# Optimization experiments

Measured on AMD Instinct MI355X. Metric: run time of the kernel, lower is better.

Reference implementation:

```python
import jax, jax.numpy as jnp
import numpy as np

B, T, N, E = 4, 8, 3000, 12000
D = 256; H = 256; HEADS = 8; DH = H // HEADS; F = 8; L = 3; HD = 64
NEG_SLOPE = 0.2


def layer_norm(x, g, b):
    m = x.mean(-1, keepdims=True)
    v = x.var(-1, keepdims=True)
    return (x - m) / jnp.sqrt(v + 1e-5) * g + b


def gat(x, edge_emb, src, dst, W, We, a_src, a_dst, a_edge):
    # x: [B,N,Din], edge_emb: [B,E,H] -> [B,N,H] via edge-conditioned graph attention
    Bc, Nc = x.shape[0], x.shape[1]
    xw = (x @ W).reshape(Bc, Nc, HEADS, DH)
    ew = (edge_emb @ We).reshape(Bc, -1, HEADS, DH)
    xs = xw[:, src]  # [B,E,HEADS,DH] gather
    xd = xw[:, dst]
    logit = (xs * a_src).sum(-1) + (xd * a_dst).sum(-1) + (ew * a_edge).sum(-1)  # [B,E,HEADS]
    logit = jnp.where(logit > 0, logit, NEG_SLOPE * logit)  # leaky_relu(0.2)

    def seg_softmax(lg):  # softmax over incoming edges per dst node
        m = jax.ops.segment_max(lg, dst, num_segments=Nc)
        e = jnp.exp(lg - m[dst])
        s = jax.ops.segment_sum(e, dst, num_segments=Nc)
        return e / (s[dst] + 1e-16)

    w = jax.vmap(seg_softmax)(logit)  # [B,E,HEADS]
    msg = (xs + ew) * w[..., None]
    out = jax.vmap(lambda m_: jax.ops.segment_sum(m_, dst, num_segments=Nc))(msg)
    return out.reshape(Bc, Nc, H)


def mlp(x, w1, b1, w2, b2):
    return jax.nn.relu(x @ w1 + b1) @ w2 + b2


def setup_inputs() -> dict:
    key = jax.random.key(0)
    ks = iter(jax.random.split(key, 64))
    rn = lambda s, sc=1.0: jax.random.normal(next(ks), s, dtype=jnp.float32) * sc
    return {
        'env_emb': rn((B, T, N, D)), 'infra_emb': rn((B, T, N, D)), 'robot_emb': rn((B, T, N, D)),
        'edge_attr': rn((B, E, F)),
        'edge_index': jax.random.randint(next(ks), (2, E), 0, N),
        'wqkv': rn((D, 3 * D), 0.05), 'bqkv': jnp.zeros((3 * D,), jnp.float32),
        'wo': rn((D, D), 0.05), 'bo': jnp.zeros((D,), jnp.float32),
        'lnf_g': jnp.ones((D,), jnp.float32), 'lnf_b': jnp.zeros((D,), jnp.float32),
        'we_emb': rn((F, H), 0.1), 'be_emb': jnp.zeros((H,), jnp.float32),
        'tg_W': rn((D, H), 0.05), 'tg_We': rn((H, H), 0.05),
        'tg_asrc': rn((HEADS, DH), 0.1), 'tg_adst': rn((HEADS, DH), 0.1), 'tg_aedge': rn((HEADS, DH), 0.1),
        'w_ih': rn((H, 4 * H), 0.05), 'w_hh': rn((H, 4 * H), 0.05), 'b_lstm': jnp.zeros((4 * H,), jnp.float32),
        'g_W': rn((L, H, H), 0.05), 'g_We': rn((L, H, H), 0.05),
        'g_asrc': rn((L, HEADS, DH), 0.1), 'g_adst': rn((L, HEADS, DH), 0.1), 'g_aedge': rn((L, HEADS, DH), 0.1),
        'g_lng': jnp.ones((L, H), jnp.float32), 'g_lnb': jnp.zeros((L, H), jnp.float32),
        'hn_w1': rn((8, H, HD), 0.05), 'hn_b1': jnp.zeros((8, HD), jnp.float32),
        'hn_w2': rn((8, HD, 1), 0.05), 'hn_b2': jnp.zeros((8, 1), jnp.float32),
        'he_w1': rn((2, 2 * H, HD), 0.05), 'he_b1': jnp.zeros((2, HD), jnp.float32),
        'he_w2': rn((2, HD, 1), 0.05), 'he_b2': jnp.zeros((2, 1), jnp.float32),
    }


def reference(env_emb, infra_emb, robot_emb, edge_attr, edge_index,
              wqkv, bqkv, wo, bo, lnf_g, lnf_b, we_emb, be_emb,
              tg_W, tg_We, tg_asrc, tg_adst, tg_aedge,
              w_ih, w_hh, b_lstm,
              g_W, g_We, g_asrc, g_adst, g_aedge, g_lng, g_lnb,
              hn_w1, hn_b1, hn_w2, hn_b2, he_w1, he_b1, he_w2, he_b2):
    # --- per-timestep 3-token cross-modal self-attention, vectorized over B,T,N ---
    tokens = jnp.stack([env_emb, infra_emb, robot_emb], axis=3)  # [B,T,N,3,D]
    qkv = tokens @ wqkv + bqkv
    q, k, v = jnp.split(qkv, 3, axis=-1)
    sh = tokens.shape[:-1] + (HEADS, DH)
    q = q.reshape(sh); k = k.reshape(sh); v = v.reshape(sh)
    att = jax.nn.softmax(jnp.einsum('btnqhd,btnkhd->btnhqk', q, k) / np.sqrt(DH).astype(np.float32), axis=-1)
    o = jnp.einsum('btnhqk,btnkhd->btnqhd', att, v).reshape(tokens.shape)
    fused_seq = layer_norm((o @ wo + bo).mean(axis=3), lnf_g, lnf_b)  # [B,T,N,D]

    edge_emb = jax.nn.relu(edge_attr @ we_emb + be_emb)  # [B,E,H]
    src = edge_index[0]; dst = edge_index[1]

    # --- TemporalGNNCell: GAT message passing feeding an LSTM cell, scanned over T ---
    def step(carry, x_t):
        h, c = carry
        m = gat(x_t, edge_emb, src, dst, tg_W, tg_We, tg_asrc, tg_adst, tg_aedge)
        gates = m @ w_ih + h @ w_hh + b_lstm
        i, f, g, oo = jnp.split(gates, 4, axis=-1)
        c = jax.nn.sigmoid(f) * c + jax.nn.sigmoid(i) * jnp.tanh(g)
        h = jax.nn.sigmoid(oo) * jnp.tanh(c)
        return (h, c), None

    z = jnp.zeros((B, N, H), fused_seq.dtype)
    (h, _), _ = jax.lax.scan(step, (z, z), jnp.moveaxis(fused_seq, 1, 0))

    # --- stacked residual GAT layers with LayerNorm ---
    for i in range(L):
        h_new = gat(h, edge_emb, src, dst, g_W[i], g_We[i], g_asrc[i], g_adst[i], g_aedge[i])
        h = layer_norm(h + h_new, g_lng[i], g_lnb[i])

    # --- prediction heads ---
    failure = jax.nn.sigmoid(mlp(h, hn_w1[0], hn_b1[0], hn_w2[0], hn_b2[0]))
    timing = jax.nn.softplus(mlp(h, hn_w1[1], hn_b1[1], hn_w2[1], hn_b2[1]))
    others = [mlp(h, hn_w1[j], hn_b1[j], hn_w2[j], hn_b2[j]) for j in range(2, 6)]  # voltage, angle, temperature, reactive
    risk = jax.nn.sigmoid(mlp(h, hn_w1[6], hn_b1[6], hn_w2[6], hn_b2[6]))
    node_out = jnp.concatenate([failure, timing] + others + [risk], axis=-1)  # [B,N,7]
    h_global = h.mean(axis=1, keepdims=True)
    freq = mlp(h_global, hn_w1[7], hn_b1[7], hn_w2[7], hn_b2[7]).reshape(B, 1)
    ef = jnp.concatenate([h[:, src], h[:, dst]], axis=-1)  # [B,E,2H]
    line = mlp(ef, he_w1[0], he_b1[0], he_w2[0], he_b2[0])
    active = mlp(ef, he_w1[1], he_b1[1], he_w2[1], he_b2[1])
    return jnp.concatenate([node_out.reshape(B, -1), line.reshape(B, -1), active.reshape(B, -1), freq], axis=1)
```

## Files before the change

kernel.cpp:

```cpp
#include <hip/hip_runtime.h>
#include <hip/hip_bf16.h>
#include <math.h>

#define DEV __device__ __forceinline__

namespace {
constexpr int B_ = 4, T_ = 8, N_ = 3000, E_ = 12000;
constexpr int OUTS_ = 45001;
}

using f32x4 = __attribute__((ext_vector_type(4))) float;
using bf16x8 = __attribute__((ext_vector_type(8))) short;

DEV float sigm_(float x) { return 1.0f / (1.0f + expf(-x)); }
DEV float softplus_(float x) { return fmaxf(x, 0.0f) + log1pf(expf(-fabsf(x))); }
DEV float wred_(float v) {
  #pragma unroll
  for (int o = 32; o > 0; o >>= 1) v += __shfl_xor(v, o, 64);
  return v;
}
DEV unsigned short f2bf(float x) {
  unsigned u = __float_as_uint(x);
  return (unsigned short)((u + 0x7FFFu + ((u >> 16) & 1u)) >> 16);
}
DEV unsigned f2bf2(float a, float b) {
  return (unsigned)f2bf(a) | ((unsigned)f2bf(b) << 16);
}
DEV float bfl(unsigned u) { return __uint_as_float(u << 16); }
DEV float bfh(unsigned u) { return __uint_as_float(u & 0xffff0000u); }

__global__ void wtb_k(const float* __restrict__ W, unsigned short* __restrict__ Wt,
                      int K, int N, int total)
{
  const int idx = blockIdx.x * blockDim.x + threadIdx.x;
  if (idx >= total) return;
  const int kn = K * N;
  const int l = idx / kn;
  const int r = idx - l * kn;
  const int k = r / N, n = r - k * N;
  Wt[(size_t)l * kn + (size_t)n * K + k] = f2bf(W[idx]);
}

__global__ void wtp_k(const float* __restrict__ W, unsigned short* __restrict__ Wt,
                      int kOff)
{
  const int idx = blockIdx.x * blockDim.x + threadIdx.x;
  if (idx >= 256 * 1024) return;
  const int k = idx >> 10;
  const int n = idx & 1023;
  const int newcol = (n & 255) * 4 + (n >> 8);
  Wt[(size_t)newcol * 512 + kOff + k] = f2bf(W[idx]);
}

__global__ void hist_k(const int* __restrict__ dst, int* __restrict__ deg)
{
  const int e = blockIdx.x * blockDim.x + threadIdx.x;
  if (e < E_) atomicAdd(&deg[dst[e]], 1);
}

__global__ __launch_bounds__(256) void scan_k(const int* __restrict__ deg,
                                              int* __restrict__ roff)
{
  __shared__ int part[256];
  const int t = threadIdx.x;
  int loc[12];
  int s = 0;
  #pragma unroll
  for (int i = 0; i < 12; ++i) {
    const int n = t * 12 + i;
    loc[i] = s;
    s += (n < N_) ? deg[n] : 0;
  }
  part[t] = s;
  __syncthreads();
  if (t == 0) {
    int run = 0;
    for (int i = 0; i < 256; ++i) { const int v = part[i]; part[i] = run; run += v; }
  }
  __syncthreads();
  const int base = part[t];
  #pragma unroll
  for (int i = 0; i < 12; ++i) {
    const int n = t * 12 + i;
    if (n < N_) roff[n] = base + loc[i];
  }
  if (t == 0) roff[N_] = E_;
}

__global__ __launch_bounds__(256) void fill_k(const int* __restrict__ dst,
                                              const int* __restrict__ roff,
                                              int* __restrict__ eord)
{
  const int n = blockIdx.x * 4 + (threadIdx.x >> 6);
  if (n >= N_) return;
  const int lane = threadIdx.x & 63;
  const unsigned long long ltm = (1ull << lane) - 1ull;
  int cnt = roff[n];
  for (int c = 0; c < E_; c += 64) {
    const int e = c + lane;
    const bool m = (e < E_) && (dst[e] == n);
    const unsigned long long mask = __ballot(m);
    if (m) eord[cnt + __popcll(mask & ltm)] = e;
    cnt += __popcll(mask);
  }
}

__global__ __launch_bounds__(256) void gemm_bfa_k(
    const unsigned short* __restrict__ A, const unsigned short* __restrict__ Wt,
    const float* __restrict__ bias, void* __restrict__ Cv,
    int M, int N, int K, int lda, int flags)
{
  __shared__ unsigned short Al[128 * 40];
  __shared__ unsigned short Bl[64 * 40];
  const int tid = threadIdx.x;
  const int bm = blockIdx.y * 128;
  const int bn = blockIdx.x * 64;
  const int lane = tid & 63;
  const int wv = tid >> 6;
  const int wm = (wv >> 1) * 64;
  const int wn = (wv & 1) * 32;
  const int s_row = tid >> 1;
  const int s_cb = (tid & 1) * 16;
  const int grow = bm + s_row;
  const unsigned short* Arow = (grow < M) ? A + (size_t)grow * lda : nullptr;
  const int b_col = tid >> 2;
  const int b_ks = (tid & 3) * 8;
  const unsigned short* Wrow = Wt + (size_t)(bn + b_col) * K + b_ks;

  f32x4 acc[4][2] = {};
  const int l15 = lane & 15;
  const int lk = (lane >> 4) * 8;

  for (int k0 = 0; k0 < K; k0 += 32) {
    uint4 a0, a1;
    if (Arow) {
      a0 = *(const uint4*)(Arow + k0 + s_cb);
      a1 = *(const uint4*)(Arow + k0 + s_cb + 8);
    } else {
      a0 = make_uint4(0, 0, 0, 0);
      a1 = a0;
    }
    *(uint4*)&Al[s_row * 40 + s_cb] = a0;
    *(uint4*)&Al[s_row * 40 + s_cb + 8] = a1;
    *(uint4*)&Bl[b_col * 40 + b_ks] = *(const uint4*)(Wrow + k0);
    __syncthreads();
    bf16x8 af[4], bfr[2];
    #pragma unroll
    for (int m = 0; m < 4; ++m)
      af[m] = *(const bf16x8*)&Al[(wm + m * 16 + l15) * 40 + lk];
    #pragma unroll
    for (int n = 0; n < 2; ++n)
      bfr[n] = *(const bf16x8*)&Bl[(wn + n * 16 + l15) * 40 + lk];
    #pragma unroll
    for (int m = 0; m < 4; ++m)
      #pragma unroll
      for (int n = 0; n < 2; ++n)
        acc[m][n] = __builtin_amdgcn_mfma_f32_16x16x32_bf16(af[m], bfr[n], acc[m][n], 0, 0, 0);
    __syncthreads();
  }
  float* Cf = (float*)Cv;
  unsigned short* Cb = (unsigned short*)Cv;
  const int r4 = (lane >> 4) * 4;
  #pragma unroll
  for (int m = 0; m < 4; ++m) {
    #pragma unroll
    for (int n = 0; n < 2; ++n) {
      const int col = bn + wn + n * 16 + l15;
      const float bv = bias ? bias[col] : 0.f;
      #pragma unroll
      for (int r = 0; r < 4; ++r) {
        const int row = bm + wm + m * 16 + r4 + r;
        if (row >= M) continue;
        float v = acc[m][n][r] + bv;
        const size_t ci = (size_t)row * N + col;
        if (flags & 1) v += Cf[ci];
        if (flags & 2) v = fmaxf(v, 0.f);
        if (flags & 4) Cb[ci] = f2bf(v);
        else Cf[ci] = v;
      }
    }
  }
}

__global__ __launch_bounds__(256) void gemm_qkv_k(
    const float* __restrict__ env, const float* __restrict__ infra,
    const float* __restrict__ robot, const unsigned short* __restrict__ Wt,
    const float* __restrict__ bias, unsigned short* __restrict__ Cb,
    int M, int nodeBase)
{
  __shared__ unsigned short Al[128 * 40];
  __shared__ unsigned short Bl[64 * 40];
  const int tid = threadIdx.x;
  const int bm = blockIdx.y * 128;
  const int bn = blockIdx.x * 64;
  const int lane = tid & 63;
  const int wv = tid >> 6;
  const int wm = (wv >> 1) * 64;
  const int wn = (wv & 1) * 32;
  const int s_row = tid >> 1;
  const int s_cb = (tid & 1) * 16;
  const int grow = bm + s_row;
  const float* Arow = nullptr;
  if (grow < M) {
    const int slot = grow % 3;
    const int node = nodeBase + grow / 3;
    const float* srcp = (slot == 0 ? env : (slot == 1 ? infra : robot));
    Arow = srcp + (size_t)node * 256;
  }
  const int b_col = tid >> 2;
  const int b_ks = (tid & 3) * 8;
  const unsigned short* Wrow = Wt + (size_t)(bn + b_col) * 256 + b_ks;

  f32x4 acc[4][2] = {};
  const int l15 = lane & 15;
  const int lk = (lane >> 4) * 8;

  for (int k0 = 0; k0 < 256; k0 += 32) {
    unsigned abuf[8];
    if (Arow) {
      const float* p = Arow + k0 + s_cb;
      #pragma unroll
      for (int i = 0; i < 4; ++i) {
        const float4 v = *(const float4*)(p + i * 4);
        abuf[i * 2 + 0] = f2bf2(v.x, v.y);
        abuf[i * 2 + 1] = f2bf2(v.z, v.w);
      }
    } else {
      #pragma unroll
      for (int i = 0; i < 8; ++i) abuf[i] = 0;
    }
    *(uint4*)&Al[s_row * 40 + s_cb] = *(uint4*)&abuf[0];
    *(uint4*)&Al[s_row * 40 + s_cb + 8] = *(uint4*)&abuf[4];
    *(uint4*)&Bl[b_col * 40 + b_ks] = *(const uint4*)(Wrow + k0);
    __syncthreads();
    bf16x8 af[4], bfr[2];
    #pragma unroll
    for (int m = 0; m < 4; ++m)
      af[m] = *(const bf16x8*)&Al[(wm + m * 16 + l15) * 40 + lk];
    #pragma unroll
    for (int n = 0; n < 2; ++n)
      bfr[n] = *(const bf16x8*)&Bl[(wn + n * 16 + l15) * 40 + lk];
    #pragma unroll
    for (int m = 0; m < 4; ++m)
      #pragma unroll
      for (int n = 0; n < 2; ++n)
        acc[m][n] = __builtin_amdgcn_mfma_f32_16x16x32_bf16(af[m], bfr[n], acc[m][n], 0, 0, 0);
    __syncthreads();
  }
  const int r4 = (lane >> 4) * 4;
  #pragma unroll
  for (int m = 0; m < 4; ++m) {
    #pragma unroll
    for (int n = 0; n < 2; ++n) {
      const int col = bn + wn + n * 16 + l15;
      const float bv = bias[col];
      #pragma unroll
      for (int r = 0; r < 4; ++r) {
        const int row = bm + wm + m * 16 + r4 + r;
        if (row >= M) continue;
        Cb[(size_t)row * 768 + col] = f2bf(acc[m][n][r] + bv);
      }
    }
  }
}

__global__ __launch_bounds__(256) void gemm_lstm_k(
    const unsigned short* __restrict__ gatall, const unsigned short* __restrict__ hbIn,
    const unsigned short* __restrict__ Wt, const float* __restrict__ b_lstm,
    float* __restrict__ h, float* __restrict__ c, unsigned short* __restrict__ hbOut,
    int t)
{
  __shared__ float Gl[128][65];
  unsigned short* Al = (unsigned short*)&Gl[0][0];
  unsigned short* Bl = Al + 128 * 40;
  const int tid = threadIdx.x;
  const int bm = blockIdx.y * 128;
  const int bn = blockIdx.x * 64;
  const int lane = tid & 63;
  const int wv = tid >> 6;
  const int wm = (wv >> 1) * 64;
  const int wn = (wv & 1) * 32;
  const int s_row = tid >> 1;
  const int s_cb = (tid & 1) * 16;
  const int grow = bm + s_row;
  const unsigned short* Arow1 = nullptr;
  const unsigned short* Arow2 = nullptr;
  if (grow < 12000) {
    const int phys = (grow / N_) * (T_ * N_) + t * N_ + (grow % N_);
    Arow1 = gatall + (size_t)phys * 256;
    Arow2 = hbIn + (size_t)grow * 256;
  }
  const int b_col = tid >> 2;
  const int b_ks = (tid & 3) * 8;
  const unsigned short* Wrow = Wt + (size_t)(bn + b_col) * 512 + b_ks;

  f32x4 acc[4][2] = {};
  const int l15 = lane & 15;
  const int lk = (lane >> 4) * 8;

  for (int k0 = 0; k0 < 512; k0 += 32) {
    uint4 a0, a1;
    if (Arow1) {
      const unsigned short* p = (k0 < 256) ? (Arow1 + k0 + s_cb)
                                           : (Arow2 + (k0 - 256) + s_cb);
      a0 = *(const uint4*)p;
      a1 = *(const uint4*)(p + 8);
    } else {
      a0 = make_uint4(0, 0, 0, 0);
      a1 = a0;
    }
    *(uint4*)&Al[s_row * 40 + s_cb] = a0;
    *(uint4*)&Al[s_row * 40 + s_cb + 8] = a1;
    *(uint4*)&Bl[b_col * 40 + b_ks] = *(const uint4*)(Wrow + k0);
    __syncthreads();
    bf16x8 af[4], bfr[2];
    #pragma unroll
    for (int m = 0; m < 4; ++m)
      af[m] = *(const bf16x8*)&Al[(wm + m * 16 + l15) * 40 + lk];
    #pragma unroll
    for (int n = 0; n < 2; ++n)
      bfr[n] = *(const bf16x8*)&Bl[(wn + n * 16 + l15) * 40 + lk];
    #pragma unroll
    for (int m = 0; m < 4; ++m)
      #pragma unroll
      for (int n = 0; n < 2; ++n)
        acc[m][n] = __builtin_amdgcn_mfma_f32_16x16x32_bf16(af[m], bfr[n], acc[m][n], 0, 0, 0);
    __syncthreads();
  }
  const int r4 = (lane >> 4) * 4;
  #pragma unroll
  for (int m = 0; m < 4; ++m)
    #pragma unroll
    for (int n = 0; n < 2; ++n) {
      const int col = wn + n * 16 + l15;
      #pragma unroll
      for (int r = 0; r < 4; ++r)
        Gl[wm + m * 16 + r4 + r][col] = acc[m][n][r];
    }
  __syncthreads();
  const int fl = lane & 7;
  const int rg = lane >> 3;
  const int dg = ((bn + wn) >> 2) + fl;
  const float bi = b_lstm[dg];
  const float bff = b_lstm[256 + dg];
  const float bg = b_lstm[512 + dg];
  const float bo = b_lstm[768 + dg];
  const int colb = wn + fl * 4;
  #pragma unroll
  for (int i = 0; i < 8; ++i) {
    const int rl = rg + i * 8;
    const int row = bm + wm + rl;
    if (row >= 12000) continue;
    const float g0 = Gl[wm + rl][colb + 0] + bi;
    const float g1 = Gl[wm + rl][colb + 1] + bff;
    const float g2 = Gl[wm + rl][colb + 2] + bg;
    const float g3 = Gl[wm + rl][colb + 3] + bo;
    const size_t idx = (size_t)row * 256 + dg;
    const float cn = sigm_(g1) * c[idx] + sigm_(g0) * tanhf(g2);
    c[idx] = cn;
    const float hn = sigm_(g3) * tanhf(cn);
    h[idx] = hn;
    hbOut[idx] = f2bf(hn);
  }
}

__global__ __launch_bounds__(256) void gemm_k(
    const float* __restrict__ A, const float* __restrict__ W,
    const float* __restrict__ bias, void* __restrict__ Cv,
    int M, int N, int K, int lda, int flags)
{
  __shared__ float As[16][68];
  __shared__ float Ws[16][64];
  const int tid = threadIdx.x;
  const int bm = blockIdx.y * 64;
  const int bn = blockIdx.x * 64;
  const int tx = tid & 15;
  const int ty = tid >> 4;
  const int ar = tid >> 2;
  const int ac = (tid & 3) << 2;
  const int wr = tid >> 4;
  const int wc = (tid & 15) << 2;
  const int grow = bm + ar;
  const float* Arow = (grow < M) ? A + (size_t)grow * lda : nullptr;
  float acc[4][4] = {};
  for (int k0 = 0; k0 < K; k0 += 16) {
    float4 av = make_float4(0.f, 0.f, 0.f, 0.f);
    if (Arow) {
      av.x = (k0 + ac + 0 < K) ? Arow[k0 + ac + 0] : 0.f;
      av.y = (k0 + ac + 1 < K) ? Arow[k0 + ac + 1] : 0.f;
      av.z = (k0 + ac + 2 < K) ? Arow[k0 + ac + 2] : 0.f;
      av.w = (k0 + ac + 3 < K) ? Arow[k0 + ac + 3] : 0.f;
    }
    As[ac + 0][ar] = av.x;
    As[ac + 1][ar] = av.y;
    As[ac + 2][ar] = av.z;
    As[ac + 3][ar] = av.w;
    float4 wv = make_float4(0.f, 0.f, 0.f, 0.f);
    if (k0 + wr < K) {
      const int gc = bn + wc;
      const float* wp = W + (size_t)(k0 + wr) * N + gc;
      wv.x = (gc + 0 < N) ? wp[0] : 0.f;
      wv.y = (gc + 1 < N) ? wp[1] : 0.f;
      wv.z = (gc + 2 < N) ? wp[2] : 0.f;
      wv.w = (gc + 3 < N) ? wp[3] : 0.f;
    }
    *(float4*)&Ws[wr][wc] = wv;
    __syncthreads();
    #pragma unroll
    for (int kk = 0; kk < 16; ++kk) {
      const float4 a = *(const float4*)&As[kk][ty << 2];
      const float4 b = *(const float4*)&Ws[kk][tx << 2];
      acc[0][0] += a.x * b.x; acc[0][1] += a.x * b.y; acc[0][2] += a.x * b.z; acc[0][3] += a.x * b.w;
      acc[1][0] += a.y * b.x; acc[1][1] += a.y * b.y; acc[1][2] += a.y * b.z; acc[1][3] += a.y * b.w;
      acc[2][0] += a.z * b.x; acc[2][1] += a.z * b.y; acc[2][2] += a.z * b.z; acc[2][3] += a.z * b.w;
      acc[3][0] += a.w * b.x; acc[3][1] += a.w * b.y; acc[3][2] += a.w * b.z; acc[3][3] += a.w * b.w;
    }
    __syncthreads();
  }
  float* Cf = (float*)Cv;
  unsigned short* Cb = (unsigned short*)Cv;
  #pragma unroll
  for (int i = 0; i < 4; ++i) {
    const int row = bm + (ty << 2) + i;
    if (row >= M) continue;
    #pragma unroll
    for (int j = 0; j < 4; ++j) {
      const int col = bn + (tx << 2) + j;
      if (col >= N) continue;
      float v = acc[i][j];
      if (bias) v += bias[col];
      if (flags & 2) v = fmaxf(v, 0.f);
      const size_t ci = (size_t)row * N + col;
      if (flags & 4) Cb[ci] = f2bf(v);
      else Cf[ci] = v;
    }
  }
}

__global__ __launch_bounds__(256) void attn_avg_k(
    const unsigned short* __restrict__ qkv,
    unsigned short* __restrict__ obar, int nodes)
{
  const int node = blockIdx.x * 4 + (threadIdx.x >> 6);
  if (node >= nodes) return;
  const int lane = threadIdx.x & 63;
  const unsigned short* base = qkv + (size_t)node * 2304 + lane * 4;
  float qv[3][4], kv[3][4], vv[3][4];
  #pragma unroll
  for (int s = 0; s < 3; ++s) {
    const uint2 uq = *(const uint2*)(base + s * 768);
    const uint2 uk = *(const uint2*)(base + s * 768 + 256);
    const uint2 uv = *(const uint2*)(base + s * 768 + 512);
    qv[s][0] = bfl(uq.x); qv[s][1] = bfh(uq.x); qv[s][2] = bfl(uq.y); qv[s][3] = bfh(uq.y);
    kv[s][0] = bfl(uk.x); kv[s][1] = bfh(uk.x); kv[s][2] = bfl(uk.y); kv[s][3] = bfh(uk.y);
    vv[s][0] = bfl(uv.x); vv[s][1] = bfh(uv.x); vv[s][2] = bfl(uv.y); vv[s][3] = bfh(uv.y);
  }
  float att[3][3];
  #pragma unroll
  for (int s = 0; s < 3; ++s) {
    #pragma unroll
    for (int t = 0; t < 3; ++t) {
      float d = qv[s][0] * kv[t][0] + qv[s][1] * kv[t][1]
              + qv[s][2] * kv[t][2] + qv[s][3] * kv[t][3];
      d += __shfl_xor(d, 1, 64);
      d += __shfl_xor(d, 2, 64);
      d += __shfl_xor(d, 4, 64);
      att[s][t] = d * 0.17677669529663687f;
    }
  }
  float cs[3] = {0.f, 0.f, 0.f};
  #pragma unroll
  for (int s = 0; s < 3; ++s) {
    const float m = fmaxf(att[s][0], fmaxf(att[s][1], att[s][2]));
    const float e0 = expf(att[s][0] - m);
    const float e1 = expf(att[s][1] - m);
    const float e2 = expf(att[s][2] - m);
    const float inv = (1.f / 3.f) / (e0 + e1 + e2);
    cs[0] += e0 * inv; cs[1] += e1 * inv; cs[2] += e2 * inv;
  }
  float o0 = cs[0] * vv[0][0] + cs[1] * vv[1][0] + cs[2] * vv[2][0];
  float o1 = cs[0] * vv[0][1] + cs[1] * vv[1][1] + cs[2] * vv[2][1];
  float o2 = cs[0] * vv[0][2] + cs[1] * vv[1][2] + cs[2] * vv[2][2];
  float o3 = cs[0] * vv[0][3] + cs[1] * vv[1][3] + cs[2] * vv[2][3];
  uint2 ob;
  ob.x = f2bf2(o0, o1);
  ob.y = f2bf2(o2, o3);
  *(uint2*)(obar + (size_t)node * 256 + lane * 4) = ob;
}

__global__ __launch_bounds__(64) void ln_k(
    const unsigned short* __restrict__ in, const float* __restrict__ g,
    const float* __restrict__ bta, unsigned short* __restrict__ outp)
{
  const int row = blockIdx.x;
  const int d0 = threadIdx.x << 2;
  const uint2 a = *(const uint2*)(in + (size_t)row * 256 + d0);
  float x[4] = { bfl(a.x), bfh(a.x), bfl(a.y), bfh(a.y) };
  float s = x[0] + x[1] + x[2] + x[3];
  s = wred_(s);
  const float mean = s * (1.f / 256.f);
  float vs = 0.f;
  #pragma unroll
  for (int i = 0; i < 4; ++i) { const float dd = x[i] - mean; vs += dd * dd; }
  vs = wred_(vs);
  const float inv = 1.0f / sqrtf(vs * (1.f / 256.f) + 1e-5f);
  const float4 gv = *(const float4*)(g + d0);
  const float4 bv = *(const float4*)(bta + d0);
  uint2 o;
  o.x = f2bf2((x[0] - mean) * inv * gv.x + bv.x, (x[1] - mean) * inv * gv.y + bv.y);
  o.y = f2bf2((x[2] - mean) * inv * gv.z + bv.z, (x[3] - mean) * inv * gv.w + bv.w);
  *(uint2*)(outp + (size_t)row * 256 + d0) = o;
}

__global__ void alphas_k(const unsigned short* __restrict__ xw, const float* __restrict__ as,
                         const float* __restrict__ ad, float* __restrict__ sal,
                         float* __restrict__ dal, int rows)
{
  const int idx = blockIdx.x * blockDim.x + threadIdx.x;
  if (idx >= rows * 8) return;
  const int row = idx >> 3, h = idx & 7;
  const unsigned short* x = xw + (size_t)row * 256 + h * 32;
  const float* a1 = as + h * 32;
  const float* a2 = ad + h * 32;
  float s = 0.f, d = 0.f;
  #pragma unroll
  for (int i = 0; i < 4; ++i) {
    const uint4 ux = *(const uint4*)(x + i * 8);
    const unsigned* p = &ux.x;
    #pragma unroll
    for (int j = 0; j < 4; ++j) {
      const float lo = bfl(p[j]), hi = bfh(p[j]);
      s += lo * a1[i * 8 + 2 * j] + hi * a1[i * 8 + 2 * j + 1];
      d += lo * a2[i * 8 + 2 * j] + hi * a2[i * 8 + 2 * j + 1];
    }
  }
  sal[idx] = s; dal[idx] = d;
}

__global__ void elog4_k(const unsigned short* __restrict__ ew,
                        const float* __restrict__ tg_ae, const float* __restrict__ g_ae,
                        float* __restrict__ el)
{
  const int idx = blockIdx.x * blockDim.x + threadIdx.x;
  if (idx >= 4 * 48000 * 8) return;
  const int l = idx / (48000 * 8);
  const int r = idx - l * (48000 * 8);
  const int row = r >> 3, h = r & 7;
  const unsigned short* x = ew + (size_t)row * 1024 + l * 256 + h * 32;
  const float* a1 = (l == 0 ? tg_ae : g_ae + (l - 1) * 256) + h * 32;
  float s = 0.f;
  #pragma unroll
  for (int i = 0; i < 4; ++i) {
    const uint4 ux = *(const uint4*)(x + i * 8);
    const unsigned* p = &ux.x;
    #pragma unroll
    for (int j = 0; j < 4; ++j) {
      s += bfl(p[j]) * a1[i * 8 + 2 * j] + bfh(p[j]) * a1[i * 8 + 2 * j + 1];
    }
  }
  el[l * 384000 + r] = s;
}

template<int OUTBF>
__global__ __launch_bounds__(256) void gat_k(
    const unsigned short* __restrict__ xw, const unsigned short* __restrict__ ew,
    const float* __restrict__ sal, const float* __restrict__ dal,
    const float* __restrict__ el, const int* __restrict__ roff,
    const int* __restrict__ eord, const int* __restrict__ srcArr,
    void* __restrict__ outp, int nwaves, int tshift, int ewStride, int ewOff)
{
  const int wid = blockIdx.x * 4 + (threadIdx.x >> 6);
  if (wid >= nwaves) return;
  const int beta = wid / N_;
  const int n = wid - beta * N_;
  const int b = beta >> tshift;
  const int lane = threadIdx.x & 63;
  const int h = lane >> 3;
  const int d0 = lane << 2;
  const float dal_h = dal[(size_t)wid * 8 + h];
  const int p0 = roff[n], p1 = roff[n + 1];
  float m = -1e30f, s = 0.f;
  float4 acc = make_float4(0.f, 0.f, 0.f, 0.f);
  for (int p = p0; p < p1; ++p) {
    const int e = eord[p];
    const int sc = srcArr[e];
    float lg = sal[((size_t)beta * N_ + sc) * 8 + h] + dal_h + el[((size_t)b * E_ + e) * 8 + h];
    lg = lg > 0.f ? lg : 0.2f * lg;
    const float mn = fmaxf(m, lg);
    const float scale = expf(m - mn);
    const float w = expf(lg - mn);
    s = s * scale + w;
    const uint2 ux = *(const uint2*)(xw + ((size_t)beta * N_ + sc) * 256 + d0);
    const uint2 ue = *(const uint2*)(ew + ((size_t)(b * E_ + e)) * ewStride + ewOff + d0);
    acc.x = acc.x * scale + w * (bfl(ux.x) + bfl(ue.x));
    acc.y = acc.y * scale + w * (bfh(ux.x) + bfh(ue.x));
    acc.z = acc.z * scale + w * (bfl(ux.y) + bfl(ue.y));
    acc.w = acc.w * scale + w * (bfh(ux.y) + bfh(ue.y));
    m = mn;
  }
  const float inv = 1.0f / (s + 1e-16f);
  if (OUTBF) {
    uint2 o;
    o.x = f2bf2(acc.x * inv, acc.y * inv);
    o.y = f2bf2(acc.z * inv, acc.w * inv);
    *(uint2*)((unsigned short*)outp + (size_t)wid * 256 + d0) = o;
  } else {
    *(float4*)((float*)outp + (size_t)wid * 256 + d0) =
        make_float4(acc.x * inv, acc.y * inv, acc.z * inv, acc.w * inv);
  }
}

__global__ __launch_bounds__(64) void resln_k(float* __restrict__ h,
                                              const float* __restrict__ add,
                                              const float* __restrict__ g,
                                              const float* __restrict__ bta,
                                              unsigned short* __restrict__ hb)
{
  const int row = blockIdx.x;
  const int d0 = threadIdx.x << 2;
  float* hp = h + (size_t)row * 256;
  const float4 hv = *(const float4*)(hp + d0);
  const float4 av = *(const float4*)(add + (size_t)row * 256 + d0);
  float x[4] = { hv.x + av.x, hv.y + av.y, hv.z + av.z, hv.w + av.w };
  float s = x[0] + x[1] + x[2] + x[3];
  s = wred_(s);
  const float mean = s * (1.f / 256.f);
  float vs = 0.f;
  #pragma unroll
  for (int i = 0; i < 4; ++i) { const float dd = x[i] - mean; vs += dd * dd; }
  vs = wred_(vs);
  const float inv = 1.0f / sqrtf(vs * (1.f / 256.f) + 1e-5f);
  const float4 gv = *(const float4*)(g + d0);
  const float4 bv = *(const float4*)(bta + d0);
  float o0 = (x[0] - mean) * inv * gv.x + bv.x;
  float o1 = (x[1] - mean) * inv * gv.y + bv.y;
  float o2 = (x[2] - mean) * inv * gv.z + bv.z;
  float o3 = (x[3] - mean) * inv * gv.w + bv.w;
  *(float4*)(hp + d0) = make_float4(o0, o1, o2, o3);
  uint2 ob;
  ob.x = f2bf2(o0, o1);
  ob.y = f2bf2(o2, o3);
  *(uint2*)(hb + (size_t)row * 256 + d0) = ob;
}

__global__ void nh2_k(const float* __restrict__ hidden, const float* __restrict__ w2,
                      const float* __restrict__ b2, float* __restrict__ outp)
{
  const int idx = blockIdx.x * blockDim.x + threadIdx.x;
  if (idx >= B_ * N_ * 7) return;
  const int row = idx / 7, j = idx % 7;
  const float* hp = hidden + (size_t)row * 448 + j * 64;
  const float* wp = w2 + j * 64;
  float a = 0.f;
  #pragma unroll
  for (int u = 0; u < 64; ++u) a += hp[u] * wp[u];
  a += b2[j];
  if (j == 0 || j == 6) a = sigm_(a);
  else if (j == 1) a = softplus_(a);
  const int b = row / N_, n = row % N_;
  outp[(size_t)b * OUTS_ + n * 7 + j] = a;
}

__global__ __launch_bounds__(256) void hglob1_k(const float* __restrict__ h,
                                                float* __restrict__ hgp)
{
  const int b = blockIdx.x;
  const int seg = blockIdx.y;
  const int d = threadIdx.x;
  float s = 0.f;
  const int n0 = seg * 120;
  for (int n = n0; n < n0 + 120; ++n)
    s += h[((size_t)(b * N_ + n)) * 256 + d];
  hgp[((size_t)(b * 25 + seg)) * 256 + d] = s;
}

__global__ __launch_bounds__(256) void hglob2_k(const float* __restrict__ hgp,
                                                float* __restrict__ hg)
{
  const int b = blockIdx.x;
  const int d = threadIdx.x;
  float s = 0.f;
  for (int i = 0; i < 25; ++i) s += hgp[((size_t)(b * 25 + i)) * 256 + d];
  hg[b * 256 + d] = s * (1.f / (float)N_);
}

__global__ __launch_bounds__(64) void freq_k(const float* __restrict__ hg,
                                             const float* __restrict__ w1, const float* __restrict__ b1,
                                             const float* __restrict__ w2, const float* __restrict__ b2,
                                             float* __restrict__ outp)
{
  const int b = blockIdx.x;
  const int u = threadIdx.x;
  float a = b1[u];
  for (int k = 0; k < 256; ++k) a += hg[b * 256 + k] * w1[k * 64 + u];
  a = fmaxf(a, 0.f) * w2[u];
  a = wred_(a);
  if (u == 0) outp[(size_t)b * OUTS_ + 45000] = a + b2[0];
}

__global__ void ef_k(const unsigned short* __restrict__ hb, const int* __restrict__ src,
                     const int* __restrict__ dst, unsigned short* __restrict__ ef)
{
  const int idx = blockIdx.x * blockDim.x + threadIdx.x;
  if (idx >= B_ * E_ * 64) return;
  const int q = idx & 63;
  const int row = idx >> 6;
  const int b = row / E_, e = row % E_;
  const int d = q << 3;
  const unsigned short* p = (d < 256)
      ? hb + ((size_t)(b * N_ + src[e])) * 256 + d
      : hb + ((size_t)(b * N_ + dst[e])) * 256 + (d - 256);
  *(uint4*)(ef + (size_t)row * 512 + d) = *(const uint4*)p;
}

__global__ void eh2_k(const float* __restrict__ hidden, const float* __restrict__ w2,
                      const float* __restrict__ b2, float* __restrict__ outp)
{
  const int idx = blockIdx.x * blockDim.x + threadIdx.x;
  if (idx >= 2 * B_ * E_) return;
  const int jj = idx / (B_ * E_);
  const int r = idx - jj * (B_ * E_);
  const int b = r / E_, e = r % E_;
  const float* hp = hidden + (size_t)r * 128 + jj * 64;
  const float* wp = w2 + jj * 64;
  float a = 0.f;
  #pragma unroll
  for (int u = 0; u < 64; ++u) a += hp[u] * wp[u];
  a += b2[jj];
  outp[(size_t)b * OUTS_ + 21000 + jj * 12000 + e] = a;
}

extern "C" void kernel_launch(void* const* d_in, const int* in_sizes, int n_in,
                              void* d_out, int out_size, void* d_ws, size_t ws_size,
                              hipStream_t stream)
{
  const float* env      = (const float*)d_in[0];
  const float* infra    = (const float*)d_in[1];
  const float* robot    = (const float*)d_in[2];
  const float* edgeattr = (const float*)d_in[3];
  const int*   eidx     = (const int*)d_in[4];
  const float* wqkv     = (const float*)d_in[5];
  const float* bqkv     = (const float*)d_in[6];
  const float* wo       = (const float*)d_in[7];
  const float* bo       = (const float*)d_in[8];
  const float* lnf_g    = (const float*)d_in[9];
  const float* lnf_b    = (const float*)d_in[10];
  const float* we_emb   = (const float*)d_in[11];
  const float* be_emb   = (const float*)d_in[12];
  const float* tg_W     = (const float*)d_in[13];
  const float* tg_We    = (const float*)d_in[14];
  const float* tg_asrc  = (const float*)d_in[15];
  const float* tg_adst  = (const float*)d_in[16];
  const float* tg_aedge = (const float*)d_in[17];
  const float* w_ih     = (const float*)d_in[18];
  const float* w_hh     = (const float*)d_in[19];
  const float* b_lstm   = (const float*)d_in[20];
  const float* g_W      = (const float*)d_in[21];
  const float* g_We     = (const float*)d_in[22];
  const float* g_asrc   = (const float*)d_in[23];
  const float* g_adst   = (const float*)d_in[24];
  const float* g_aedge  = (const float*)d_in[25];
  const float* g_lng    = (const float*)d_in[26];
  const float* g_lnb    = (const float*)d_in[27];
  const float* hn_w1    = (const float*)d_in[28];
  const float* hn_b1    = (const float*)d_in[29];
  const float* hn_w2    = (const float*)d_in[30];
  const float* hn_b2    = (const float*)d_in[31];
  const float* he_w1    = (const float*)d_in[32];
  const float* he_b1    = (const float*)d_in[33];
  const float* he_w2    = (const float*)d_in[34];
  const float* he_b2    = (const float*)d_in[35];

  const int* src = eidx;
  const int* dst = eidx + E_;
  float* outp = (float*)d_out;
  float* ws = (float*)d_ws;

  unsigned short* wtb0 = (unsigned short*)ws;
  unsigned short* wt_qkv  = wtb0;
  unsigned short* wt_wo   = wtb0 + 196608;
  unsigned short* wt_tgW  = wtb0 + 262144;
  unsigned short* wt_tgWe = wtb0 + 327680;
  unsigned short* wt_gWe  = wtb0 + 393216;
  unsigned short* wt_lstm = wtb0 + 589824;
  unsigned short* wt_gW   = wtb0 + 1114112;
  unsigned short* wt_hn   = wtb0 + 1310720;
  unsigned short* wt_he   = wtb0 + 1425408;

  const size_t D0 = 1600000;
  unsigned short* qkvb  = (unsigned short*)(ws + D0);
  unsigned short* tmpAb = (unsigned short*)(ws + D0 + 13824000);
  unsigned short* obarb = (unsigned short*)(ws + D0 + 38400000);
  unsigned short* fseqb = (unsigned short*)(ws + D0 + 50688000);
  unsigned short* xwallb  = (unsigned short*)(ws + D0);
  unsigned short* gatallb = (unsigned short*)(ws + D0 + 12288000);
  unsigned short* eembb   = (unsigned short*)(ws + D0 + 24576000);
  float* h  = ws + D0 + 30720000;
  float* c  = ws + D0 + 33792000;
  unsigned short* hb0 = (unsigned short*)(ws + D0 + 36864000);
  unsigned short* hb1 = (unsigned short*)(ws + D0 + 38400000);
  unsigned short* ewall = (unsigned short*)(ws + D0 + 62976000);
  float* elogall = ws + D0 + 87552000;
  float* sal     = ws + D0 + 89088000;
  float* dal     = ws + D0 + 89856000;
  int* ideg  = (int*)(ws + D0 + 90624000);
  int* iroff = ideg + 3008;
  int* ieord = iroff + 3008;
  float* hg  = ws + D0 + 90650000;
  float* hgp = ws + D0 + 90652048;
  unsigned short* xw_sb = (unsigned short*)(ws + D0 + 40000000);
  float* gat_s = ws + D0 + 41600000;
  float* hidn = ws + D0;
  unsigned short* efb = (unsigned short*)(ws + D0 + 5376000);
  float* hide = ws + D0 + 17664000;

  auto mgemm = [&](const unsigned short* A, const unsigned short* Wt, const float* bias,
                   void* C, int M, int N, int K, int lda, int flags) {
    dim3 grid(N / 64, (M + 127) / 128);
    gemm_bfa_k<<<grid, dim3(256), 0, stream>>>(A, Wt, bias, C, M, N, K, lda, flags);
  };
  auto cvtb = [&](const float* W, unsigned short* Wt, int K, int N, int L) {
    const int total = K * N * L;
    wtb_k<<<(total + 255) / 256, 256, 0, stream>>>(W, Wt, K, N, total);
  };

  cvtb(wqkv, wt_qkv, 256, 768, 1);
  cvtb(wo, wt_wo, 256, 256, 1);
  cvtb(tg_W, wt_tgW, 256, 256, 1);
  cvtb(tg_We, wt_tgWe, 256, 256, 1);
  cvtb(g_We, wt_gWe, 256, 256, 3);
  wtp_k<<<1024, 256, 0, stream>>>(w_ih, wt_lstm, 0);
  wtp_k<<<1024, 256, 0, stream>>>(w_hh, wt_lstm, 256);
  cvtb(g_W, wt_gW, 256, 256, 3);
  cvtb(hn_w1, wt_hn, 256, 64, 7);
  cvtb(he_w1, wt_he, 512, 64, 2);

  hipMemsetAsync(ideg, 0, 3000 * sizeof(int), stream);
  hist_k<<<(E_ + 255) / 256, 256, 0, stream>>>(dst, ideg);
  scan_k<<<1, 256, 0, stream>>>(ideg, iroff);
  fill_k<<<750, 256, 0, stream>>>(dst, iroff, ieord);

  for (int chunk = 0; chunk < 8; ++chunk) {
    dim3 grid(768 / 64, (36000 + 127) / 128);
    gemm_qkv_k<<<grid, dim3(256), 0, stream>>>(env, infra, robot, wt_qkv, bqkv,
                                               qkvb, 36000, chunk * 12000);
    attn_avg_k<<<3000, 256, 0, stream>>>(qkvb, obarb + (size_t)chunk * 12000 * 256, 12000);
  }
  mgemm(obarb, wt_wo, bo, tmpAb, 96000, 256, 256, 256, 4);
  ln_k<<<96000, 64, 0, stream>>>(tmpAb, lnf_g, lnf_b, fseqb);

  {
    dim3 grid(4, 750);
    gemm_k<<<grid, dim3(256), 0, stream>>>(edgeattr, we_emb, be_emb, eembb,
                                           48000, 256, 8, 8, 2 | 4);
  }
  mgemm(eembb, wt_tgWe, nullptr, ewall, 48000, 1024, 256, 256, 4);
  elog4_k<<<6000, 256, 0, stream>>>(ewall, tg_aedge, g_aedge, elogall);

  mgemm(fseqb, wt_tgW, nullptr, xwallb, 96000, 256, 256, 256, 4);
  alphas_k<<<3000, 256, 0, stream>>>(xwallb, tg_asrc, tg_adst, sal, dal, 96000);
  gat_k<1><<<24000, 256, 0, stream>>>(xwallb, ewall, sal, dal, elogall, iroff, ieord,
                                      src, gatallb, 96000, 3, 1024, 0);

  hipMemsetAsync(c, 0, 12288000, stream);
  hipMemsetAsync(hb0, 0, 6144000, stream);
  unsigned short* hbq[2] = { hb0, hb1 };
  for (int t = 0; t < T_; ++t) {
    dim3 grid(16, 94);
    gemm_lstm_k<<<grid, dim3(256), 0, stream>>>(gatallb, hbq[t & 1], wt_lstm, b_lstm,
                                                h, c, hbq[(t + 1) & 1], t);
  }
  unsigned short* hbf = hbq[0];

  for (int l = 0; l < 3; ++l) {
    mgemm(hbf, wt_gW + (size_t)l * 65536, nullptr, xw_sb, 12000, 256, 256, 256, 4);
    alphas_k<<<375, 256, 0, stream>>>(xw_sb, g_asrc + l * 256, g_adst + l * 256, sal, dal, 12000);
    gat_k<0><<<3000, 256, 0, stream>>>(xw_sb, ewall, sal, dal, elogall + 384000 * (l + 1),
                                       iroff, ieord, src, gat_s, 12000, 0,
                                       1024, 256 * (l + 1));
    resln_k<<<12000, 64, 0, stream>>>(h, gat_s, g_lng + l * 256, g_lnb + l * 256, hbf);
  }

  mgemm(hbf, wt_hn, hn_b1, hidn, 12000, 448, 256, 256, 2);
  nh2_k<<<(84000 + 255) / 256, 256, 0, stream>>>(hidn, hn_w2, hn_b2, outp);

  hglob1_k<<<dim3(4, 25), 256, 0, stream>>>(h, hgp);
  hglob2_k<<<4, 256, 0, stream>>>(hgp, hg);
  freq_k<<<4, 64, 0, stream>>>(hg, hn_w1 + 7 * 16384, hn_b1 + 7 * 64,
                               hn_w2 + 7 * 64, hn_b2 + 7, outp);

  ef_k<<<12000, 256, 0, stream>>>(hbf, src, dst, efb);
  mgemm(efb, wt_he, he_b1, hide, 48000, 128, 512, 512, 2);
  eh2_k<<<(96000 + 255) / 256, 256, 0, stream>>>(hide, he_w2, he_b2, outp);
}
```

Measured before the change: 1.682 ms.

## Fuse edge-feature gather into GEMM, skip zero LSTM step, halve QKV chunks

The edge head now gathers src/dst node rows directly inside a new MFMA GEMM kernel with ReLU epilogue, removing the ef_k materialization of a 48000x512 buffer and its reread. The first LSTM step skips the recurrent half of K since h0 is zero, which also lets the hb0 memset be dropped. The QKV/attention loop processes 24000 rows per chunk in 4 iterations instead of 8, with workspace buffers re-laid out so tmpAb aliases the qkv scratch. This reduces launches and memory traffic at the cost of more workspace per chunk and reliance on the new aliasing being safe.

```diff
diff --git a/kernel.cpp b/kernel.cpp
--- a/kernel.cpp
+++ b/kernel.cpp
@@ -268,7 +268,7 @@
     const unsigned short* __restrict__ gatall, const unsigned short* __restrict__ hbIn,
     const unsigned short* __restrict__ Wt, const float* __restrict__ b_lstm,
     float* __restrict__ h, float* __restrict__ c, unsigned short* __restrict__ hbOut,
-    int t)
+    int t, int kEnd)
 {
   __shared__ float Gl[128][65];
   unsigned short* Al = (unsigned short*)&Gl[0][0];
@@ -298,7 +298,7 @@
   const int l15 = lane & 15;
   const int lk = (lane >> 4) * 8;
 
-  for (int k0 = 0; k0 < 512; k0 += 32) {
+  for (int k0 = 0; k0 < kEnd; k0 += 32) {
     uint4 a0, a1;
     if (Arow1) {
       const unsigned short* p = (k0 < 256) ? (Arow1 + k0 + s_cb)
@@ -361,6 +361,85 @@
     const float hn = sigm_(g3) * tanhf(cn);
     h[idx] = hn;
     hbOut[idx] = f2bf(hn);
+  }
+}
+
+__global__ __launch_bounds__(256) void gemm_ef_k(
+    const unsigned short* __restrict__ hb, const int* __restrict__ srcA,
+    const int* __restrict__ dstA, const unsigned short* __restrict__ Wt,
+    const float* __restrict__ bias, float* __restrict__ Cf)
+{
+  __shared__ unsigned short Al[128 * 40];
+  __shared__ unsigned short Bl[64 * 40];
+  const int tid = threadIdx.x;
+  const int bm = blockIdx.y * 128;
+  const int bn = blockIdx.x * 64;
+  const int lane = tid & 63;
+  const int wv = tid >> 6;
+  const int wm = (wv >> 1) * 64;
+  const int wn = (wv & 1) * 32;
+  const int s_row = tid >> 1;
+  const int s_cb = (tid & 1) * 16;
+  const int grow = bm + s_row;
+  const unsigned short* Arow1 = nullptr;
+  const unsigned short* Arow2 = nullptr;
+  if (grow < 48000) {
+    const int b = grow / E_;
+    const int e = grow - b * E_;
+    Arow1 = hb + ((size_t)(b * N_ + srcA[e])) * 256;
+    Arow2 = hb + ((size_t)(b * N_ + dstA[e])) * 256;
+  }
+  const int b_col = tid >> 2;
+  const int b_ks = (tid & 3) * 8;
+  const unsigned short* Wrow = Wt + (size_t)(bn + b_col) * 512 + b_ks;
+
+  f32x4 acc[4][2] = {};
+  const int l15 = lane & 15;
+  const int lk = (lane >> 4) * 8;
+
+  for (int k0 = 0; k0 < 512; k0 += 32) {
+    uint4 a0, a1;
+    if (Arow1) {
+      const unsigned short* p = (k0 < 256) ? (Arow1 + k0 + s_cb)
+                                           : (Arow2 + (k0 - 256) + s_cb);
+      a0 = *(const uint4*)p;
+      a1 = *(const uint4*)(p + 8);
+    } else {
+      a0 = make_uint4(0, 0, 0, 0);
+      a1 = a0;
+    }
+    *(uint4*)&Al[s_row * 40 + s_cb] = a0;
+    *(uint4*)&Al[s_row * 40 + s_cb + 8] = a1;
+    *(uint4*)&Bl[b_col * 40 + b_ks] = *(const uint4*)(Wrow + k0);
+    __syncthreads();
+    bf16x8 af[4], bfr[2];
+    #pragma unroll
+    for (int m = 0; m < 4; ++m)
+      af[m] = *(const bf16x8*)&Al[(wm + m * 16 + l15) * 40 + lk];
+    #pragma unroll
+    for (int n = 0; n < 2; ++n)
+      bfr[n] = *(const bf16x8*)&Bl[(wn + n * 16 + l15) * 40 + lk];
+    #pragma unroll
+    for (int m = 0; m < 4; ++m)
+      #pragma unroll
+      for (int n = 0; n < 2; ++n)
+        acc[m][n] = __builtin_amdgcn_mfma_f32_16x16x32_bf16(af[m], bfr[n], acc[m][n], 0, 0, 0);
+    __syncthreads();
+  }
+  const int r4 = (lane >> 4) * 4;
+  #pragma unroll
+  for (int m = 0; m < 4; ++m) {
+    #pragma unroll
+    for (int n = 0; n < 2; ++n) {
+      const int col = bn + wn + n * 16 + l15;
+      const float bv = bias[col];
+      #pragma unroll
+      for (int r = 0; r < 4; ++r) {
+        const int row = bm + wm + m * 16 + r4 + r;
+        if (row >= 48000) continue;
+        Cf[(size_t)row * 128 + col] = fmaxf(acc[m][n][r] + bv, 0.f);
+      }
+    }
   }
 }
 
@@ -696,21 +775,6 @@
   a = fmaxf(a, 0.f) * w2[u];
   a = wred_(a);
   if (u == 0) outp[(size_t)b * OUTS_ + 45000] = a + b2[0];
-}
-
-__global__ void ef_k(const unsigned short* __restrict__ hb, const int* __restrict__ src,
-                     const int* __restrict__ dst, unsigned short* __restrict__ ef)
-{
-  const int idx = blockIdx.x * blockDim.x + threadIdx.x;
-  if (idx >= B_ * E_ * 64) return;
-  const int q = idx & 63;
-  const int row = idx >> 6;
-  const int b = row / E_, e = row % E_;
-  const int d = q << 3;
-  const unsigned short* p = (d < 256)
-      ? hb + ((size_t)(b * N_ + src[e])) * 256 + d
-      : hb + ((size_t)(b * N_ + dst[e])) * 256 + (d - 256);
-  *(uint4*)(ef + (size_t)row * 512 + d) = *(const uint4*)p;
 }
 
 __global__ void eh2_k(const float* __restrict__ hidden, const float* __restrict__ w2,
@@ -789,9 +853,9 @@
 
   const size_t D0 = 1600000;
   unsigned short* qkvb  = (unsigned short*)(ws + D0);
-  unsigned short* tmpAb = (unsigned short*)(ws + D0 + 13824000);
-  unsigned short* obarb = (unsigned short*)(ws + D0 + 38400000);
-  unsigned short* fseqb = (unsigned short*)(ws + D0 + 50688000);
+  unsigned short* tmpAb = qkvb;
+  unsigned short* obarb = (unsigned short*)(ws + D0 + 27648000);
+  unsigned short* fseqb = (unsigned short*)(ws + D0 + 39936000);
   unsigned short* xwallb  = (unsigned short*)(ws + D0);
   unsigned short* gatallb = (unsigned short*)(ws + D0 + 12288000);
   unsigned short* eembb   = (unsigned short*)(ws + D0 + 24576000);
@@ -811,7 +875,6 @@
   unsigned short* xw_sb = (unsigned short*)(ws + D0 + 40000000);
   float* gat_s = ws + D0 + 41600000;
   float* hidn = ws + D0;
-  unsigned short* efb = (unsigned short*)(ws + D0 + 5376000);
   float* hide = ws + D0 + 17664000;
 
   auto mgemm = [&](const unsigned short* A, const unsigned short* Wt, const float* bias,
@@ -840,11 +903,11 @@
   scan_k<<<1, 256, 0, stream>>>(ideg, iroff);
   fill_k<<<750, 256, 0, stream>>>(dst, iroff, ieord);
 
-  for (int chunk = 0; chunk < 8; ++chunk) {
-    dim3 grid(768 / 64, (36000 + 127) / 128);
+  for (int chunk = 0; chunk < 4; ++chunk) {
+    dim3 grid(768 / 64, (72000 + 127) / 128);
     gemm_qkv_k<<<grid, dim3(256), 0, stream>>>(env, infra, robot, wt_qkv, bqkv,
-                                               qkvb, 36000, chunk * 12000);
-    attn_avg_k<<<3000, 256, 0, stream>>>(qkvb, obarb + (size_t)chunk * 12000 * 256, 12000);
+                                               qkvb, 72000, chunk * 24000);
+    attn_avg_k<<<6000, 256, 0, stream>>>(qkvb, obarb + (size_t)chunk * 24000 * 256, 24000);
   }
   mgemm(obarb, wt_wo, bo, tmpAb, 96000, 256, 256, 256, 4);
   ln_k<<<96000, 64, 0, stream>>>(tmpAb, lnf_g, lnf_b, fseqb);
@@ -863,12 +926,12 @@
                                       src, gatallb, 96000, 3, 1024, 0);
 
   hipMemsetAsync(c, 0, 12288000, stream);
-  hipMemsetAsync(hb0, 0, 6144000, stream);
   unsigned short* hbq[2] = { hb0, hb1 };
   for (int t = 0; t < T_; ++t) {
     dim3 grid(16, 94);
     gemm_lstm_k<<<grid, dim3(256), 0, stream>>>(gatallb, hbq[t & 1], wt_lstm, b_lstm,
-                                                h, c, hbq[(t + 1) & 1], t);
+                                                h, c, hbq[(t + 1) & 1], t,
+                                                t == 0 ? 256 : 512);
   }
   unsigned short* hbf = hbq[0];
 
@@ -889,7 +952,9 @@
   freq_k<<<4, 64, 0, stream>>>(hg, hn_w1 + 7 * 16384, hn_b1 + 7 * 64,
                                hn_w2 + 7 * 64, hn_b2 + 7, outp);
 
-  ef_k<<<12000, 256, 0, stream>>>(hbf, src, dst, efb);
-  mgemm(efb, wt_he, he_b1, hide, 48000, 128, 512, 512, 2);
+  {
+    dim3 grid(2, 375);
+    gemm_ef_k<<<grid, dim3(256), 0, stream>>>(hbf, src, dst, wt_he, he_b1, hide);
+  }
   eh2_k<<<(96000 + 255) / 256, 256, 0, stream>>>(hide, he_w2, he_b2, outp);
 }
```

New measurement: 1.627 ms. 1.03x faster.
